# Kernel optimization log

Hardware: AMD Instinct MI355X
Metric: run time of the kernel (lower is better)

Reference implementation:

```python
import jax, jax.numpy as jnp
import jax.scipy.linalg as jsp
import numpy as np

# Problem dimensions (match init_kwargs P_shape/A_shape)
N = 256   # variables
M = 512   # constraints
B = 64    # batch

# OSQP ADMM hyper-parameters (fixed-rho variant of the OSQP algorithm)
SIGMA = 1e-6
RHO = 0.1
ALPHA = 1.6
N_ITERS = 500


def setup_inputs() -> dict:
    key = jax.random.key(0)
    kP, kq, kA, kc = jax.random.split(key, 4)
    # P is diagonal with strictly positive entries -> PSD (values are the nnz of P)
    P_val = jax.random.uniform(kP, (B, N), dtype=jnp.float32) + 0.1
    q_val = jax.random.normal(kq, (B, N), dtype=jnp.float32)
    # A is a dense pattern; values stored row-major as its nnz vector
    A_val = jax.random.normal(kA, (B, M * N), dtype=jnp.float32) / np.sqrt(N)
    # Feasible box: l <= u by construction
    center = jax.random.normal(kc, (B, M), dtype=jnp.float32)
    l_val = center - 1.0
    u_val = center + 1.0
    return {"P_val": P_val, "q_val": q_val, "A_val": A_val, "l_val": l_val, "u_val": u_val}


def _admm_qp(P_val, q_val, A_val, l_val, u_val):
    """Batched OSQP-style ADMM solve of min 1/2 x'Px + q'x  s.t. l <= Ax <= u.

    P is diagonal (nnz pattern = diag), A is dense (nnz pattern = full m x n).
    """
    A = A_val.reshape(B, M, N)                      # [B,m,n]
    # KKT-like matrix M_k = P + sigma*I + rho*A'A   [B,n,n]
    eye = jnp.eye(N, dtype=P_val.dtype)
    P_diag = P_val + SIGMA                          # diagonal of P + sigma*I
    Mk = RHO * jnp.einsum('bmi,bmj->bij', A, A) + jax.vmap(jnp.diag)(P_diag)
    L = jnp.linalg.cholesky(Mk)                     # [B,n,n], factor once, reuse
    Lt = jnp.swapaxes(L, -1, -2)

    def kkt_solve(rhs):                             # rhs [B,n]
        y1 = jsp.solve_triangular(L, rhs[..., None], lower=True)
        y2 = jsp.solve_triangular(Lt, y1, lower=False)
        return y2[..., 0]

    x0 = jnp.zeros((B, N), dtype=P_val.dtype)
    z0 = jnp.zeros((B, M), dtype=P_val.dtype)
    y0 = jnp.zeros((B, M), dtype=P_val.dtype)

    def step(state, _):
        x, z, y = state
        rhs = SIGMA * x - q_val + jnp.einsum('bmn,bm->bn', A, RHO * z - y)
        x_t = kkt_solve(rhs)                        # x-tilde
        z_t = jnp.einsum('bmn,bn->bm', A, x_t)      # z-tilde = A x_t
        x_new = ALPHA * x_t + (1.0 - ALPHA) * x
        z_hat = ALPHA * z_t + (1.0 - ALPHA) * z
        z_new = jnp.clip(z_hat + y / RHO, l_val, u_val)
        y_new = y + RHO * (z_hat - z_new)
        return (x_new, z_new, y_new), None

    (x, _, _), _ = jax.lax.scan(step, (x0, z0, y0), None, length=N_ITERS)
    return x


def reference(P_val, q_val, A_val, l_val, u_val):
    return _admm_qp(P_val, q_val, A_val, l_val, u_val)   # [B, n] primal solutions
```

## Files before the change

### kernel.cpp

```cpp
#include <hip/hip_runtime.h>
#include <hip/hip_fp16.h>

#define N_VAR 256
#define M_CON 512
#define BATCH 64
#define SIGMA_C 1e-6f
#define RHO_C 0.1f
#define ALPHA_C 1.6f
#define NITERS 500

typedef _Float16 f16x8 __attribute__((ext_vector_type(8)));
typedef float f32x4 __attribute__((ext_vector_type(4)));

__global__ __launch_bounds__(256) void k_transpose(const float* __restrict__ A,
                                                   float* __restrict__ At) {
  __shared__ float tile[32][33];
  int b = blockIdx.z;
  int n0 = blockIdx.x * 32;
  int m0 = blockIdx.y * 32;
  const float* Ab = A + (size_t)b * (M_CON * N_VAR);
  float* Atb = At + (size_t)b * (M_CON * N_VAR);
  int tx = threadIdx.x, ty = threadIdx.y;
#pragma unroll
  for (int j = 0; j < 32; j += 8)
    tile[ty + j][tx] = Ab[(size_t)(m0 + ty + j) * N_VAR + n0 + tx];
  __syncthreads();
#pragma unroll
  for (int j = 0; j < 32; j += 8)
    Atb[(size_t)(n0 + ty + j) * M_CON + m0 + tx] = tile[tx][ty + j];
}

__global__ __launch_bounds__(256) void k_ntgemm(
    const float* __restrict__ X, const float* __restrict__ Y,
    float* __restrict__ C, float* __restrict__ C2, int I, int J, int K,
    long long bsX, long long bsY, long long bsC, float alpha,
    const float* __restrict__ diagv, int tilesJ, int packC) {
  int b = blockIdx.y;
  int ti = blockIdx.x / tilesJ, tj = blockIdx.x % tilesJ;
  int i0 = ti * 128, j0 = tj * 128;
  const float* Xb = X + (size_t)b * bsX;
  const float* Yb = Y + (size_t)b * bsY;
  __shared__ float Xs[16][128];
  __shared__ float Ys[16][128];
  int tid = threadIdx.x;
  int tx = tid & 15, ty = tid >> 4;
  float acc[8][8];
#pragma unroll
  for (int r = 0; r < 8; ++r)
#pragma unroll
    for (int c = 0; c < 8; ++c) acc[r][c] = 0.0f;

  for (int kk = 0; kk < K; kk += 16) {
#pragma unroll
    for (int v = 0; v < 2; ++v) {
      int idx = v * 256 + tid;
      int row = idx >> 2;
      int k4 = (idx & 3) * 4;
      float4 gx = *(const float4*)(Xb + (size_t)(i0 + row) * K + kk + k4);
      Xs[k4 + 0][row] = gx.x; Xs[k4 + 1][row] = gx.y;
      Xs[k4 + 2][row] = gx.z; Xs[k4 + 3][row] = gx.w;
      float4 gy = *(const float4*)(Yb + (size_t)(j0 + row) * K + kk + k4);
      Ys[k4 + 0][row] = gy.x; Ys[k4 + 1][row] = gy.y;
      Ys[k4 + 2][row] = gy.z; Ys[k4 + 3][row] = gy.w;
    }
    __syncthreads();
#pragma unroll
    for (int k = 0; k < 16; ++k) {
      float xr[8], yr[8];
      *(float4*)&xr[0] = *(float4*)&Xs[k][ty * 8];
      *(float4*)&xr[4] = *(float4*)&Xs[k][ty * 8 + 4];
      *(float4*)&yr[0] = *(float4*)&Ys[k][tx * 8];
      *(float4*)&yr[4] = *(float4*)&Ys[k][tx * 8 + 4];
#pragma unroll
      for (int r = 0; r < 8; ++r)
#pragma unroll
        for (int c = 0; c < 8; ++c) acc[r][c] += xr[r] * yr[c];
    }
    __syncthreads();
  }
  if (packC == 2) {
    unsigned* Ch = (unsigned*)C + (size_t)b * 65536;
    unsigned* Ce = (unsigned*)C2 + (size_t)b * 65536;
#pragma unroll
    for (int r = 0; r < 8; ++r) {
      int gi = i0 + ty * 8 + r;
#pragma unroll
      for (int c = 0; c < 8; c += 2) {
        int gj = j0 + tx * 8 + c;
        float v0 = acc[r][c] * alpha, v1 = acc[r][c + 1] * alpha;
        __half2 hh = __floats2half2_rn(v0, v1);
        float2 fb = __half22float2(hh);
        __half2 he = __floats2half2_rn((v0 - fb.x) * 256.0f,
                                       (v1 - fb.y) * 256.0f);
        int idx = gi * 128 + (gj >> 1);
        Ch[idx] = *(unsigned*)&hh;
        Ce[idx] = *(unsigned*)&he;
      }
    }
    return;
  }
  float* Cb = C + (size_t)b * bsC;
#pragma unroll
  for (int r = 0; r < 8; ++r) {
    int gi = i0 + ty * 8 + r;
#pragma unroll
    for (int c = 0; c < 8; ++c) {
      int gj = j0 + tx * 8 + c;
      float val = acc[r][c] * alpha;
      if (diagv != nullptr && gi == gj) val += diagv[(size_t)b * N_VAR + gi] + SIGMA_C;
      Cb[(size_t)gi * J + gj] = val;
    }
  }
}

__global__ __launch_bounds__(256) void k_cast_split(
    const float* __restrict__ in, unsigned* __restrict__ oh,
    unsigned* __restrict__ oe, int n4) {
  int i = blockIdx.x * 256 + threadIdx.x;
  if (i >= n4) return;
  float4 v = ((const float4*)in)[i];
  __half2 h01 = __floats2half2_rn(v.x, v.y);
  __half2 h23 = __floats2half2_rn(v.z, v.w);
  float2 f01 = __half22float2(h01);
  float2 f23 = __half22float2(h23);
  __half2 e01 = __floats2half2_rn((v.x - f01.x) * 256.0f, (v.y - f01.y) * 256.0f);
  __half2 e23 = __floats2half2_rn((v.z - f23.x) * 256.0f, (v.w - f23.y) * 256.0f);
  uint2 uh; uh.x = *(unsigned*)&h01; uh.y = *(unsigned*)&h23;
  uint2 ue; ue.x = *(unsigned*)&e01; ue.y = *(unsigned*)&e23;
  ((uint2*)oh)[i] = uh;
  ((uint2*)oe)[i] = ue;
}

__global__ __launch_bounds__(256, 4) void k_mfma_g(
    const _Float16* __restrict__ Fh, const _Float16* __restrict__ Fe,
    const _Float16* __restrict__ Ah, const _Float16* __restrict__ Ae,
    unsigned* __restrict__ Gp) {
  int b = blockIdx.y;
  int bx = blockIdx.x;
  int t = threadIdx.x, l = t & 63, wv = t >> 6;
  int i0 = (bx >> 2) * 32;
  int j0 = (bx & 3) * 128 + wv * 32;
  const _Float16* Fhb = Fh + (size_t)b * 131072;
  const _Float16* Feb = Fe + (size_t)b * 131072;
  const _Float16* Ahb = Ah + (size_t)b * 131072;
  const _Float16* Aeb = Ae + (size_t)b * 131072;
  unsigned* Gpb = Gp + (size_t)b * 131072;

  int lr = l & 15, lk = (l >> 4) * 8;
  f32x4 acc00 = {0,0,0,0}, acc01 = {0,0,0,0}, acc10 = {0,0,0,0}, acc11 = {0,0,0,0};
  f32x4 ar00 = {0,0,0,0}, ar01 = {0,0,0,0}, ar10 = {0,0,0,0}, ar11 = {0,0,0,0};

  for (int kk = 0; kk < 256; kk += 32) {
    f16x8 af0 = *(const f16x8*)&Fhb[(size_t)(i0 + lr) * 256 + kk + lk];
    f16x8 af1 = *(const f16x8*)&Fhb[(size_t)(i0 + 16 + lr) * 256 + kk + lk];
    f16x8 ae0 = *(const f16x8*)&Feb[(size_t)(i0 + lr) * 256 + kk + lk];
    f16x8 ae1 = *(const f16x8*)&Feb[(size_t)(i0 + 16 + lr) * 256 + kk + lk];
    f16x8 bf0 = *(const f16x8*)&Ahb[(size_t)(j0 + lr) * 256 + kk + lk];
    f16x8 bf1 = *(const f16x8*)&Ahb[(size_t)(j0 + 16 + lr) * 256 + kk + lk];
    f16x8 be0 = *(const f16x8*)&Aeb[(size_t)(j0 + lr) * 256 + kk + lk];
    f16x8 be1 = *(const f16x8*)&Aeb[(size_t)(j0 + 16 + lr) * 256 + kk + lk];
    acc00 = __builtin_amdgcn_mfma_f32_16x16x32_f16(af0, bf0, acc00, 0, 0, 0);
    acc01 = __builtin_amdgcn_mfma_f32_16x16x32_f16(af0, bf1, acc01, 0, 0, 0);
    acc10 = __builtin_amdgcn_mfma_f32_16x16x32_f16(af1, bf0, acc10, 0, 0, 0);
    acc11 = __builtin_amdgcn_mfma_f32_16x16x32_f16(af1, bf1, acc11, 0, 0, 0);
    ar00 = __builtin_amdgcn_mfma_f32_16x16x32_f16(af0, be0, ar00, 0, 0, 0);
    ar01 = __builtin_amdgcn_mfma_f32_16x16x32_f16(af0, be1, ar01, 0, 0, 0);
    ar10 = __builtin_amdgcn_mfma_f32_16x16x32_f16(af1, be0, ar10, 0, 0, 0);
    ar11 = __builtin_amdgcn_mfma_f32_16x16x32_f16(af1, be1, ar11, 0, 0, 0);
    ar00 = __builtin_amdgcn_mfma_f32_16x16x32_f16(ae0, bf0, ar00, 0, 0, 0);
    ar01 = __builtin_amdgcn_mfma_f32_16x16x32_f16(ae0, bf1, ar01, 0, 0, 0);
    ar10 = __builtin_amdgcn_mfma_f32_16x16x32_f16(ae1, bf0, ar10, 0, 0, 0);
    ar11 = __builtin_amdgcn_mfma_f32_16x16x32_f16(ae1, bf1, ar11, 0, 0, 0);
  }

#pragma unroll
  for (int tr = 0; tr < 2; ++tr)
#pragma unroll
    for (int tc = 0; tc < 2; ++tc) {
      const f32x4* am = (tr == 0) ? ((tc == 0) ? &acc00 : &acc01)
                                  : ((tc == 0) ? &acc10 : &acc11);
      const f32x4* ae = (tr == 0) ? ((tc == 0) ? &ar00 : &ar01)
                                  : ((tc == 0) ? &ar10 : &ar11);
#pragma unroll
      for (int r = 0; r < 4; ++r) {
        float v = (*am)[r] + (*ae)[r] * (1.0f / 256.0f);
        float vp = __shfl_xor(v, 1);
        int gi = i0 + tr * 16 + (l >> 4) * 4 + r;
        int gj = j0 + tc * 16 + lr;
        if (!(l & 1)) {
          __half2 hh = __floats2half2_rn(v, vp);
          int sl = gi >> 7, rl = gi & 127;
          int t2 = ((((gj >> 7) << 1) | (rl >> 6)) << 6) | (rl & 63);
          Gpb[(size_t)sl * 32768 + ((gj & 127) >> 1) * 512 + t2] = *(unsigned*)&hh;
        }
      }
    }
}

__global__ __launch_bounds__(512, 2) void k_invert(const float* __restrict__ Mk,
                                                   float* __restrict__ Mi) {
  int b = blockIdx.x;
  const float* src = Mk + (size_t)b * 65536;
  float* dst = Mi + (size_t)b * 65536;
  int t = threadIdx.x;
  int c = t & 255, rh = t >> 8;

  float a[128];
#pragma unroll
  for (int j = 0; j < 128; ++j) a[j] = src[(size_t)(rh * 128 + j) * 256 + c];

  __shared__ float colPan[256][8];
  __shared__ float rowPan[2][8][260];
  __shared__ float PiSh[64];
  __shared__ float Rp[8][260];

  int rh_s = __builtin_amdgcn_readfirstlane(rh);
  int cw_s = __builtin_amdgcn_readfirstlane((t >> 6) & 3);

  if (rh == 0) {
#pragma unroll
    for (int j = 0; j < 8; ++j) rowPan[0][j][c] = a[j];
  }
  __syncthreads();

  for (int s = 0; s < 32; ++s) {
    int kb = s * 8;
    int cur = s & 1, nxt = cur ^ 1;
    int kh = kb >> 7, kj = kb & 127;
    int khn = (kb + 8) >> 7, kjn = (kb + 8) & 127;
    bool mycol = (c >= kb) && (c < kb + 8);

    if (cw_s == (kb >> 6)) {
      if (mycol) {
        int f = c - kb;
#pragma unroll
        for (int j = 0; j < 128; ++j) colPan[rh * 128 + j][f] = a[j];
      }
    }
    if (t < 64) {
      int e = t >> 3, f = t & 7;
      float p = rowPan[cur][e][kb + f];
#pragma unroll
      for (int k2 = 0; k2 < 8; ++k2) {
        float piv = __shfl(p, k2 * 8 + k2);
        float rv = __shfl(p, k2 * 8 + f);
        float cv = __shfl(p, e * 8 + k2);
        float pivinv = 1.0f / piv;
        float srv = rv * pivinv;
        float gen = p - cv * srv;
        p = gen;
        if (e == k2) p = srv;
        if (f == k2) p = -cv * pivinv;
        if (e == k2 && f == k2) p = pivinv;
      }
      PiSh[t] = p;
    }
    __syncthreads();

    float rpan[8];
#pragma unroll
    for (int f2 = 0; f2 < 8; ++f2) rpan[f2] = rowPan[cur][f2][c];
    float rp[8];
#pragma unroll
    for (int e = 0; e < 8; ++e) {
      float4 p0 = *(const float4*)&PiSh[e * 8];
      float4 p1 = *(const float4*)&PiSh[e * 8 + 4];
      rp[e] = p0.x * rpan[0] + p0.y * rpan[1] + p0.z * rpan[2] + p0.w * rpan[3] +
              p1.x * rpan[4] + p1.y * rpan[5] + p1.z * rpan[6] + p1.w * rpan[7];
    }
    if (cw_s == (kb >> 6)) {
      if (mycol) {
        int f = c - kb;
#pragma unroll
        for (int e = 0; e < 8; ++e) rp[e] = PiSh[e * 8 + f];
      }
    }
#pragma unroll
    for (int e = 0; e < 8; ++e) Rp[e][c] = rp[e];

    bool myhalfk = (rh_s == kh);
    bool stashw = (s != 31) && (rh_s == khn);
#pragma unroll
    for (int j = 0; j < 128; ++j) {
      float4 c0 = *(const float4*)&colPan[rh * 128 + j][0];
      float4 c1 = *(const float4*)&colPan[rh * 128 + j][4];
      float aold = a[j];
      float nv = aold -
                 (c0.x * rp[0] + c0.y * rp[1] + c0.z * rp[2] + c0.w * rp[3] +
                  c1.x * rp[4] + c1.y * rp[5] + c1.z * rp[6] + c1.w * rp[7]);
      if (mycol) nv -= aold;
      if (myhalfk && j >= kj && j < kj + 8)
        nv = Rp[j - kj][c];
      a[j] = nv;
      if (stashw && j >= kjn && j < kjn + 8)
        rowPan[nxt][j - kjn][c] = nv;
    }
    __syncthreads();
  }

#pragma unroll
  for (int j = 0; j < 128; ++j) dst[(size_t)(rh * 128 + j) * 256 + c] = a[j];
}

__global__ __launch_bounds__(256) void k_matvec_h(const float* __restrict__ Mi,
                                                  const float* __restrict__ q,
                                                  float* __restrict__ h) {
  int b = blockIdx.x, t = threadIdx.x;
  __shared__ float qs[256];
  qs[t] = q[(size_t)b * 256 + t];
  __syncthreads();
  const float* Mb = Mi + (size_t)b * 65536;
  float acc = 0.0f;
  for (int k = 0; k < 256; ++k) acc += Mb[(size_t)k * 256 + t] * qs[k];
  h[(size_t)b * 256 + t] = acc;
}

__global__ __launch_bounds__(512) void k_matvec_d(const float* __restrict__ At,
                                                  const float* __restrict__ h,
                                                  float* __restrict__ d) {
  int b = blockIdx.x, t = threadIdx.x;
  __shared__ float hs[256];
  if (t < 256) hs[t] = h[(size_t)b * 256 + t];
  __syncthreads();
  const float* Ab = At + (size_t)b * 131072;
  float acc = 0.0f;
  for (int n = 0; n < 256; ++n) acc += Ab[(size_t)n * 512 + t] * hs[n];
  d[(size_t)b * 512 + t] = acc;
}

__global__ __launch_bounds__(512) void k_admm4(
    const unsigned* __restrict__ Gpk_g, const float* __restrict__ dvec,
    const float* __restrict__ lv, const float* __restrict__ uv,
    unsigned long long* __restrict__ wtag, float* __restrict__ Sbuf) {
  int g = blockIdx.x;
  int b = (g & 7) + 8 * ((g >> 3) & 7);
  int s = g >> 6;
  int t = threadIdx.x;
  int l = t & 63, wv = t >> 6;
  int c0 = wv * 64;
  int cg = wv >> 1, hc = wv & 1;

  __shared__ __align__(16) float wbuf[8][64];
  __shared__ float part[2][8][128];

  const unsigned* gsrc =
      Gpk_g + (size_t)(b * 4 + s) * 32768 + (size_t)(hc * 32) * 512 + cg * 128 + l;

  float zreg = 0.0f, yreg = 0.0f, Sreg = 0.0f;
  float lreg = 0.0f, ureg = 0.0f, dreg = 0.0f;
  if (t < 128) {
    lreg = lv[(size_t)b * 512 + s * 128 + t];
    ureg = uv[(size_t)b * 512 + s * 128 + t];
    dreg = dvec[(size_t)b * 512 + s * 128 + t];
  }
  wbuf[wv][l] = 0.0f;

  unsigned long long* wt0 = wtag + (size_t)b * 512;
  unsigned long long* wt1 = wtag + 32768 + (size_t)b * 512;
  const float4* wq4 = (const float4*)(wbuf[wv]);

  for (int it = 0; it < NITERS; ++it) {
    unsigned gva[32], gvb[32];
#pragma unroll
    for (int k = 0; k < 32; ++k) {
      gva[k] = gsrc[(size_t)k * 512];
      gvb[k] = gsrc[(size_t)k * 512 + 64];
    }

    if (it > 0) {
      unsigned long long* wp = (it & 1) ? wt1 : wt0;
      unsigned want = (unsigned)it;
      unsigned long long v = __hip_atomic_load(&wp[c0 + l], __ATOMIC_RELAXED,
                                               __HIP_MEMORY_SCOPE_AGENT);
      bool got = ((unsigned)(v >> 32) == want);
      while (!__all(got)) {
        if (!got) {
          unsigned long long v2 = __hip_atomic_load(
              &wp[c0 + l], __ATOMIC_RELAXED, __HIP_MEMORY_SCOPE_AGENT);
          if ((unsigned)(v2 >> 32) == want) { v = v2; got = true; }
        }
      }
      wbuf[wv][l] = __uint_as_float((unsigned)(v & 0xffffffffu));
    }

    float r0a = 0.f, r0b = 0.f, r1a = 0.f, r1b = 0.f;
#pragma unroll
    for (int j = 0; j < 8; ++j) {
      float4 wa = wq4[2 * j];
      float4 wc = wq4[2 * j + 1];
      float2 fa0 = __half22float2(*(__half2*)&gva[4 * j + 0]);
      float2 fa1 = __half22float2(*(__half2*)&gva[4 * j + 1]);
      float2 fa2 = __half22float2(*(__half2*)&gva[4 * j + 2]);
      float2 fa3 = __half22float2(*(__half2*)&gva[4 * j + 3]);
      float2 fb0 = __half22float2(*(__half2*)&gvb[4 * j + 0]);
      float2 fb1 = __half22float2(*(__half2*)&gvb[4 * j + 1]);
      float2 fb2 = __half22float2(*(__half2*)&gvb[4 * j + 2]);
      float2 fb3 = __half22float2(*(__half2*)&gvb[4 * j + 3]);
      r0a += fa0.x * wa.x + fa0.y * wa.y + fa1.x * wa.z + fa1.y * wa.w;
      r0b += fa2.x * wc.x + fa2.y * wc.y + fa3.x * wc.z + fa3.y * wc.w;
      r1a += fb0.x * wa.x + fb0.y * wa.y + fb1.x * wa.z + fb1.y * wa.w;
      r1b += fb2.x * wc.x + fb2.y * wc.y + fb3.x * wc.z + fb3.y * wc.w;
    }
    int pp = it & 1;
    part[pp][wv][l] = r0a + r0b;
    part[pp][wv][64 + l] = r1a + r1b;
    __syncthreads();

    if (t < 128) {
      float w_old = RHO_C * zreg - yreg;
      Sreg = w_old - 0.6f * Sreg;
      float p = part[pp][0][t] + part[pp][1][t] + part[pp][2][t] +
                part[pp][3][t] + part[pp][4][t] + part[pp][5][t] +
                part[pp][6][t] + part[pp][7][t];
      float zt = p - dreg;
      float zh = ALPHA_C * zt + (1.0f - ALPHA_C) * zreg;
      float zc = zh + yreg * (1.0f / RHO_C);
      zc = fminf(fmaxf(zc, lreg), ureg);
      yreg += RHO_C * (zh - zc);
      zreg = zc;
      if (it < NITERS - 1) {
        float wn = RHO_C * zreg - yreg;
        unsigned long long pk =
            ((unsigned long long)(unsigned)(it + 1) << 32) |
            (unsigned long long)__float_as_uint(wn);
        unsigned long long* wp = ((it + 1) & 1) ? wt1 : wt0;
        __hip_atomic_store(&wp[s * 128 + t], pk, __ATOMIC_RELAXED,
                           __HIP_MEMORY_SCOPE_AGENT);
      }
    }
  }

  if (t < 128) Sbuf[(size_t)b * 512 + s * 128 + t] = Sreg;
}

__global__ __launch_bounds__(256) void k_final(
    const float* __restrict__ A, const float* __restrict__ q,
    const float* __restrict__ Mi, const float* __restrict__ Sbuf,
    float* __restrict__ xout) {
  int b = blockIdx.x, t = threadIdx.x;
  __shared__ float Ssh[512];
  __shared__ float uu[256];
  for (int i = t; i < 512; i += 256) Ssh[i] = Sbuf[(size_t)b * 512 + i];
  __syncthreads();
  const float* Ab = A + (size_t)b * 131072;
  float acc = 0.0f;
  for (int m = 0; m < 512; ++m) acc += Ab[(size_t)m * 256 + t] * Ssh[m];
  uu[t] = ALPHA_C * acc - q[(size_t)b * 256 + t];
  __syncthreads();
  const float* Mb = Mi + (size_t)b * 65536;
  float x = 0.0f;
  for (int kk = 0; kk < 256; ++kk) x += Mb[(size_t)kk * 256 + t] * uu[kk];
  xout[(size_t)b * 256 + t] = x;
}

extern "C" void kernel_launch(void* const* d_in, const int* in_sizes, int n_in,
                              void* d_out, int out_size, void* d_ws, size_t ws_size,
                              hipStream_t stream) {
  (void)in_sizes; (void)n_in; (void)out_size; (void)ws_size;
  const float* P = (const float*)d_in[0];
  const float* q = (const float*)d_in[1];
  const float* Av = (const float*)d_in[2];
  const float* lv = (const float*)d_in[3];
  const float* uv = (const float*)d_in[4];
  float* xout = (float*)d_out;

  float* ws = (float*)d_ws;
  float* At = ws;
  unsigned* Ah = (unsigned*)ws;
  unsigned* Ae = (unsigned*)(ws + 4194304);
  float* Mi = ws + 8388608;
  float* Mk = ws + 12582912;
  float* Gp = ws + 12582912;
  float* Fh = ws + 20971520;
  float* Fe = ws + 25165824;
  float* hv = ws + 29360128;
  float* dv = ws + 29376512;
  float* Sbuf = ws + 29409280;
  unsigned long long* wtag = (unsigned long long*)(ws + 29442048);

  hipMemsetAsync(wtag, 0, 131072 * 4, stream);

  k_transpose<<<dim3(8, 16, 64), dim3(32, 8), 0, stream>>>(Av, At);
  k_ntgemm<<<dim3(4, 64), 256, 0, stream>>>(At, At, Mk, nullptr, 256, 256, 512,
                                            131072LL, 131072LL, 65536LL,
                                            RHO_C, P, 2, 0);
  k_invert<<<64, 512, 0, stream>>>(Mk, Mi);
  k_matvec_h<<<64, 256, 0, stream>>>(Mi, q, hv);
  k_matvec_d<<<64, 512, 0, stream>>>(At, hv, dv);
  k_cast_split<<<8192, 256, 0, stream>>>(Av, Ah, Ae, 2097152);
  k_ntgemm<<<dim3(8, 64), 256, 0, stream>>>(Av, Mi, Fh, Fe, 512, 256, 256,
                                            131072LL, 65536LL, 0LL,
                                            1.0f, nullptr, 2, 2);
  k_mfma_g<<<dim3(64, 64), 256, 0, stream>>>(
      (const _Float16*)Fh, (const _Float16*)Fe,
      (const _Float16*)Ah, (const _Float16*)Ae, (unsigned*)Gp);
  k_admm4<<<256, 512, 0, stream>>>((const unsigned*)Gp, dv, lv, uv, wtag, Sbuf);
  k_final<<<64, 256, 0, stream>>>(Av, q, Mi, Sbuf, xout);
}
```

Before: 1.539 ms.

## Cache half of the G block in LDS and vectorize remaining global loads

The precomputed G matrix is split into two halves with a new per-thread contiguous layout. In the persistent ADMM kernel, one half is loaded once into 64KB of shared memory and reused across all iterations. The other half is streamed from global memory each iteration as wide uint4 loads instead of 64 scalar strided loads. This cuts per-iteration global/L2 traffic in the latency-bound loop, at the cost of large LDS usage, which limits blocks per CU.

```diff
diff --git a/kernel.cpp b/kernel.cpp
--- a/kernel.cpp
+++ b/kernel.cpp
@@ -134,7 +134,7 @@
 __global__ __launch_bounds__(256, 4) void k_mfma_g(
     const _Float16* __restrict__ Fh, const _Float16* __restrict__ Fe,
     const _Float16* __restrict__ Ah, const _Float16* __restrict__ Ae,
-    unsigned* __restrict__ Gp) {
+    unsigned* __restrict__ GA, unsigned* __restrict__ GB) {
   int b = blockIdx.y;
   int bx = blockIdx.x;
   int t = threadIdx.x, l = t & 63, wv = t >> 6;
@@ -144,7 +144,6 @@
   const _Float16* Feb = Fe + (size_t)b * 131072;
   const _Float16* Ahb = Ah + (size_t)b * 131072;
   const _Float16* Aeb = Ae + (size_t)b * 131072;
-  unsigned* Gpb = Gp + (size_t)b * 131072;
 
   int lr = l & 15, lk = (l >> 4) * 8;
   f32x4 acc00 = {0,0,0,0}, acc01 = {0,0,0,0}, acc10 = {0,0,0,0}, acc11 = {0,0,0,0};
@@ -190,8 +189,11 @@
         if (!(l & 1)) {
           __half2 hh = __floats2half2_rn(v, vp);
           int sl = gi >> 7, rl = gi & 127;
-          int t2 = ((((gj >> 7) << 1) | (rl >> 6)) << 6) | (rl & 63);
-          Gpb[(size_t)sl * 32768 + ((gj & 127) >> 1) * 512 + t2] = *(unsigned*)&hh;
+          size_t idx =
+              ((size_t)((b * 4 + sl) * 512 + (gj >> 6) * 64 + (rl & 63))) * 32 +
+              ((gj >> 1) & 31);
+          if (rl & 64) GB[idx] = *(unsigned*)&hh;
+          else         GA[idx] = *(unsigned*)&hh;
         }
       }
     }
@@ -329,22 +331,30 @@
 }
 
 __global__ __launch_bounds__(512) void k_admm4(
-    const unsigned* __restrict__ Gpk_g, const float* __restrict__ dvec,
-    const float* __restrict__ lv, const float* __restrict__ uv,
-    unsigned long long* __restrict__ wtag, float* __restrict__ Sbuf) {
+    const unsigned* __restrict__ GA, const unsigned* __restrict__ GB,
+    const float* __restrict__ dvec, const float* __restrict__ lv,
+    const float* __restrict__ uv, unsigned long long* __restrict__ wtag,
+    float* __restrict__ Sbuf) {
   int g = blockIdx.x;
   int b = (g & 7) + 8 * ((g >> 3) & 7);
   int s = g >> 6;
   int t = threadIdx.x;
   int l = t & 63, wv = t >> 6;
   int c0 = wv * 64;
-  int cg = wv >> 1, hc = wv & 1;
-
+
+  __shared__ __align__(16) unsigned Gs[16384];
   __shared__ __align__(16) float wbuf[8][64];
   __shared__ float part[2][8][128];
 
-  const unsigned* gsrc =
-      Gpk_g + (size_t)(b * 4 + s) * 32768 + (size_t)(hc * 32) * 512 + cg * 128 + l;
+  const uint4* gA =
+      (const uint4*)(GA + ((size_t)(b * 4 + s) * 512 + c0 + l) * 32);
+  const uint4* gB =
+      (const uint4*)(GB + ((size_t)(b * 4 + s) * 512 + c0 + l) * 32);
+  uint4* GsV = (uint4*)Gs;
+
+#pragma unroll
+  for (int j4 = 0; j4 < 8; ++j4)
+    GsV[(wv * 8 + j4) * 64 + l] = gA[j4];
 
   float zreg = 0.0f, yreg = 0.0f, Sreg = 0.0f;
   float lreg = 0.0f, ureg = 0.0f, dreg = 0.0f;
@@ -360,12 +370,9 @@
   const float4* wq4 = (const float4*)(wbuf[wv]);
 
   for (int it = 0; it < NITERS; ++it) {
-    unsigned gva[32], gvb[32];
-#pragma unroll
-    for (int k = 0; k < 32; ++k) {
-      gva[k] = gsrc[(size_t)k * 512];
-      gvb[k] = gsrc[(size_t)k * 512 + 64];
-    }
+    uint4 gb[8];
+#pragma unroll
+    for (int k = 0; k < 8; ++k) gb[k] = gB[k];
 
     if (it > 0) {
       unsigned long long* wp = (it & 1) ? wt1 : wt0;
@@ -388,14 +395,16 @@
     for (int j = 0; j < 8; ++j) {
       float4 wa = wq4[2 * j];
       float4 wc = wq4[2 * j + 1];
-      float2 fa0 = __half22float2(*(__half2*)&gva[4 * j + 0]);
-      float2 fa1 = __half22float2(*(__half2*)&gva[4 * j + 1]);
-      float2 fa2 = __half22float2(*(__half2*)&gva[4 * j + 2]);
-      float2 fa3 = __half22float2(*(__half2*)&gva[4 * j + 3]);
-      float2 fb0 = __half22float2(*(__half2*)&gvb[4 * j + 0]);
-      float2 fb1 = __half22float2(*(__half2*)&gvb[4 * j + 1]);
-      float2 fb2 = __half22float2(*(__half2*)&gvb[4 * j + 2]);
-      float2 fb3 = __half22float2(*(__half2*)&gvb[4 * j + 3]);
+      uint4 ga = GsV[(wv * 8 + j) * 64 + l];
+      uint4 gv = gb[j];
+      float2 fa0 = __half22float2(*(__half2*)&ga.x);
+      float2 fa1 = __half22float2(*(__half2*)&ga.y);
+      float2 fa2 = __half22float2(*(__half2*)&ga.z);
+      float2 fa3 = __half22float2(*(__half2*)&ga.w);
+      float2 fb0 = __half22float2(*(__half2*)&gv.x);
+      float2 fb1 = __half22float2(*(__half2*)&gv.y);
+      float2 fb2 = __half22float2(*(__half2*)&gv.z);
+      float2 fb3 = __half22float2(*(__half2*)&gv.w);
       r0a += fa0.x * wa.x + fa0.y * wa.y + fa1.x * wa.z + fa1.y * wa.w;
       r0b += fa2.x * wc.x + fa2.y * wc.y + fa3.x * wc.z + fa3.y * wc.w;
       r1a += fb0.x * wa.x + fb0.y * wa.y + fb1.x * wa.z + fb1.y * wa.w;
@@ -470,7 +479,8 @@
   unsigned* Ae = (unsigned*)(ws + 4194304);
   float* Mi = ws + 8388608;
   float* Mk = ws + 12582912;
-  float* Gp = ws + 12582912;
+  unsigned* GA = (unsigned*)(ws + 12582912);
+  unsigned* GB = (unsigned*)(ws + 16777216);
   float* Fh = ws + 20971520;
   float* Fe = ws + 25165824;
   float* hv = ws + 29360128;
@@ -493,7 +503,7 @@
                                             1.0f, nullptr, 2, 2);
   k_mfma_g<<<dim3(64, 64), 256, 0, stream>>>(
       (const _Float16*)Fh, (const _Float16*)Fe,
-      (const _Float16*)Ah, (const _Float16*)Ae, (unsigned*)Gp);
-  k_admm4<<<256, 512, 0, stream>>>((const unsigned*)Gp, dv, lv, uv, wtag, Sbuf);
+      (const _Float16*)Ah, (const _Float16*)Ae, GA, GB);
+  k_admm4<<<256, 512, 0, stream>>>(GA, GB, dv, lv, uv, wtag, Sbuf);
   k_final<<<64, 256, 0, stream>>>(Av, q, Mi, Sbuf, xout);
 }
```

Measured after the change: 1.641 ms. 1.07x slower.

## Replace FP32 SIMT GEMMs with split-FP16 MFMA GEMMs for setup stages

Applied to the files above, without the earlier changes.

Removes the scalar-FP32 tiled GEMM kernel and computes A'A and A*Minv with a new MFMA kernel. The kernel splits each operand into a high FP16 part and a scaled residual part, then recombines three cross products to recover near-FP32 accuracy. This adds cast-split passes over At and Mi and reshuffles workspace buffers to hold them. Separately, the ADMM loop now loads the G-matrix values inside the inner loop instead of prefetching them into 64 registers, which lowers register pressure but exposes load latency after the wait. The emulated precision may differ slightly from true FP32.

```diff
diff --git a/kernel.cpp b/kernel.cpp
--- a/kernel.cpp
+++ b/kernel.cpp
@@ -28,89 +28,6 @@
 #pragma unroll
   for (int j = 0; j < 32; j += 8)
     Atb[(size_t)(n0 + ty + j) * M_CON + m0 + tx] = tile[tx][ty + j];
-}
-
-__global__ __launch_bounds__(256) void k_ntgemm(
-    const float* __restrict__ X, const float* __restrict__ Y,
-    float* __restrict__ C, float* __restrict__ C2, int I, int J, int K,
-    long long bsX, long long bsY, long long bsC, float alpha,
-    const float* __restrict__ diagv, int tilesJ, int packC) {
-  int b = blockIdx.y;
-  int ti = blockIdx.x / tilesJ, tj = blockIdx.x % tilesJ;
-  int i0 = ti * 128, j0 = tj * 128;
-  const float* Xb = X + (size_t)b * bsX;
-  const float* Yb = Y + (size_t)b * bsY;
-  __shared__ float Xs[16][128];
-  __shared__ float Ys[16][128];
-  int tid = threadIdx.x;
-  int tx = tid & 15, ty = tid >> 4;
-  float acc[8][8];
-#pragma unroll
-  for (int r = 0; r < 8; ++r)
-#pragma unroll
-    for (int c = 0; c < 8; ++c) acc[r][c] = 0.0f;
-
-  for (int kk = 0; kk < K; kk += 16) {
-#pragma unroll
-    for (int v = 0; v < 2; ++v) {
-      int idx = v * 256 + tid;
-      int row = idx >> 2;
-      int k4 = (idx & 3) * 4;
-      float4 gx = *(const float4*)(Xb + (size_t)(i0 + row) * K + kk + k4);
-      Xs[k4 + 0][row] = gx.x; Xs[k4 + 1][row] = gx.y;
-      Xs[k4 + 2][row] = gx.z; Xs[k4 + 3][row] = gx.w;
-      float4 gy = *(const float4*)(Yb + (size_t)(j0 + row) * K + kk + k4);
-      Ys[k4 + 0][row] = gy.x; Ys[k4 + 1][row] = gy.y;
-      Ys[k4 + 2][row] = gy.z; Ys[k4 + 3][row] = gy.w;
-    }
-    __syncthreads();
-#pragma unroll
-    for (int k = 0; k < 16; ++k) {
-      float xr[8], yr[8];
-      *(float4*)&xr[0] = *(float4*)&Xs[k][ty * 8];
-      *(float4*)&xr[4] = *(float4*)&Xs[k][ty * 8 + 4];
-      *(float4*)&yr[0] = *(float4*)&Ys[k][tx * 8];
-      *(float4*)&yr[4] = *(float4*)&Ys[k][tx * 8 + 4];
-#pragma unroll
-      for (int r = 0; r < 8; ++r)
-#pragma unroll
-        for (int c = 0; c < 8; ++c) acc[r][c] += xr[r] * yr[c];
-    }
-    __syncthreads();
-  }
-  if (packC == 2) {
-    unsigned* Ch = (unsigned*)C + (size_t)b * 65536;
-    unsigned* Ce = (unsigned*)C2 + (size_t)b * 65536;
-#pragma unroll
-    for (int r = 0; r < 8; ++r) {
-      int gi = i0 + ty * 8 + r;
-#pragma unroll
-      for (int c = 0; c < 8; c += 2) {
-        int gj = j0 + tx * 8 + c;
-        float v0 = acc[r][c] * alpha, v1 = acc[r][c + 1] * alpha;
-        __half2 hh = __floats2half2_rn(v0, v1);
-        float2 fb = __half22float2(hh);
-        __half2 he = __floats2half2_rn((v0 - fb.x) * 256.0f,
-                                       (v1 - fb.y) * 256.0f);
-        int idx = gi * 128 + (gj >> 1);
-        Ch[idx] = *(unsigned*)&hh;
-        Ce[idx] = *(unsigned*)&he;
-      }
-    }
-    return;
-  }
-  float* Cb = C + (size_t)b * bsC;
-#pragma unroll
-  for (int r = 0; r < 8; ++r) {
-    int gi = i0 + ty * 8 + r;
-#pragma unroll
-    for (int c = 0; c < 8; ++c) {
-      int gj = j0 + tx * 8 + c;
-      float val = acc[r][c] * alpha;
-      if (diagv != nullptr && gi == gj) val += diagv[(size_t)b * N_VAR + gi] + SIGMA_C;
-      Cb[(size_t)gi * J + gj] = val;
-    }
-  }
 }
 
 __global__ __launch_bounds__(256) void k_cast_split(
@@ -129,6 +46,81 @@
   uint2 ue; ue.x = *(unsigned*)&e01; ue.y = *(unsigned*)&e23;
   ((uint2*)oh)[i] = uh;
   ((uint2*)oe)[i] = ue;
+}
+
+__global__ __launch_bounds__(256, 4) void k_mfma_nt(
+    const _Float16* __restrict__ Xh, const _Float16* __restrict__ Xe,
+    const _Float16* __restrict__ Yh, const _Float16* __restrict__ Ye,
+    float* __restrict__ C0, float* __restrict__ C1,
+    int K, int jTiles, long long bsX, long long bsY, long long bsC,
+    float alpha, const float* __restrict__ diagv, int mode) {
+  int b = blockIdx.y;
+  int bx = blockIdx.x;
+  int t = threadIdx.x, l = t & 63, wv = t >> 6;
+  int i0 = (bx / jTiles) * 32;
+  int j0 = (bx % jTiles) * 128 + wv * 32;
+  const _Float16* Xhb = Xh + (size_t)b * bsX;
+  const _Float16* Xeb = Xe + (size_t)b * bsX;
+  const _Float16* Yhb = Yh + (size_t)b * bsY;
+  const _Float16* Yeb = Ye + (size_t)b * bsY;
+
+  int lr = l & 15, lk = (l >> 4) * 8;
+  f32x4 m00 = {0,0,0,0}, m01 = {0,0,0,0}, m10 = {0,0,0,0}, m11 = {0,0,0,0};
+  f32x4 c00 = {0,0,0,0}, c01 = {0,0,0,0}, c10 = {0,0,0,0}, c11 = {0,0,0,0};
+  f32x4 s00 = {0,0,0,0}, s01 = {0,0,0,0}, s10 = {0,0,0,0}, s11 = {0,0,0,0};
+
+  for (int kk = 0; kk < K; kk += 32) {
+    f16x8 xh0 = *(const f16x8*)&Xhb[(size_t)(i0 + lr) * K + kk + lk];
+    f16x8 xh1 = *(const f16x8*)&Xhb[(size_t)(i0 + 16 + lr) * K + kk + lk];
+    f16x8 xe0 = *(const f16x8*)&Xeb[(size_t)(i0 + lr) * K + kk + lk];
+    f16x8 xe1 = *(const f16x8*)&Xeb[(size_t)(i0 + 16 + lr) * K + kk + lk];
+    f16x8 yh0 = *(const f16x8*)&Yhb[(size_t)(j0 + lr) * K + kk + lk];
+    f16x8 yh1 = *(const f16x8*)&Yhb[(size_t)(j0 + 16 + lr) * K + kk + lk];
+    f16x8 ye0 = *(const f16x8*)&Yeb[(size_t)(j0 + lr) * K + kk + lk];
+    f16x8 ye1 = *(const f16x8*)&Yeb[(size_t)(j0 + 16 + lr) * K + kk + lk];
+    m00 = __builtin_amdgcn_mfma_f32_16x16x32_f16(xh0, yh0, m00, 0, 0, 0);
+    m01 = __builtin_amdgcn_mfma_f32_16x16x32_f16(xh0, yh1, m01, 0, 0, 0);
+    m10 = __builtin_amdgcn_mfma_f32_16x16x32_f16(xh1, yh0, m10, 0, 0, 0);
+    m11 = __builtin_amdgcn_mfma_f32_16x16x32_f16(xh1, yh1, m11, 0, 0, 0);
+    c00 = __builtin_amdgcn_mfma_f32_16x16x32_f16(xh0, ye0, c00, 0, 0, 0);
+    c01 = __builtin_amdgcn_mfma_f32_16x16x32_f16(xh0, ye1, c01, 0, 0, 0);
+    c10 = __builtin_amdgcn_mfma_f32_16x16x32_f16(xh1, ye0, c10, 0, 0, 0);
+    c11 = __builtin_amdgcn_mfma_f32_16x16x32_f16(xh1, ye1, c11, 0, 0, 0);
+    c00 = __builtin_amdgcn_mfma_f32_16x16x32_f16(xe0, yh0, c00, 0, 0, 0);
+    c01 = __builtin_amdgcn_mfma_f32_16x16x32_f16(xe0, yh1, c01, 0, 0, 0);
+    c10 = __builtin_amdgcn_mfma_f32_16x16x32_f16(xe1, yh0, c10, 0, 0, 0);
+    c11 = __builtin_amdgcn_mfma_f32_16x16x32_f16(xe1, yh1, c11, 0, 0, 0);
+    s00 = __builtin_amdgcn_mfma_f32_16x16x32_f16(xe0, ye0, s00, 0, 0, 0);
+    s01 = __builtin_amdgcn_mfma_f32_16x16x32_f16(xe0, ye1, s01, 0, 0, 0);
+    s10 = __builtin_amdgcn_mfma_f32_16x16x32_f16(xe1, ye0, s10, 0, 0, 0);
+    s11 = __builtin_amdgcn_mfma_f32_16x16x32_f16(xe1, ye1, s11, 0, 0, 0);
+  }
+
+#pragma unroll
+  for (int tr = 0; tr < 2; ++tr)
+#pragma unroll
+    for (int tc = 0; tc < 2; ++tc) {
+      f32x4 vm = tr ? (tc ? m11 : m10) : (tc ? m01 : m00);
+      f32x4 vc = tr ? (tc ? c11 : c10) : (tc ? c01 : c00);
+      f32x4 vs = tr ? (tc ? s11 : s10) : (tc ? s01 : s00);
+#pragma unroll
+      for (int r = 0; r < 4; ++r) {
+        float v = (vm[r] + vc[r] * (1.0f / 256.0f) +
+                   vs[r] * (1.0f / 65536.0f)) * alpha;
+        int gi = i0 + tr * 16 + (l >> 4) * 4 + r;
+        int gj = j0 + tc * 16 + lr;
+        if (mode == 0) {
+          if (diagv != nullptr && gi == gj)
+            v += diagv[(size_t)b * N_VAR + gi] + SIGMA_C;
+          C0[(size_t)b * bsC + (size_t)gi * 256 + gj] = v;
+        } else {
+          _Float16 fh = (_Float16)v;
+          _Float16 fe = (_Float16)((v - (float)fh) * 256.0f);
+          ((_Float16*)C0)[(size_t)b * bsC + (size_t)gi * 256 + gj] = fh;
+          ((_Float16*)C1)[(size_t)b * bsC + (size_t)gi * 256 + gj] = fe;
+        }
+      }
+    }
 }
 
 __global__ __launch_bounds__(256, 4) void k_mfma_g(
@@ -360,13 +352,6 @@
   const float4* wq4 = (const float4*)(wbuf[wv]);
 
   for (int it = 0; it < NITERS; ++it) {
-    unsigned gva[32], gvb[32];
-#pragma unroll
-    for (int k = 0; k < 32; ++k) {
-      gva[k] = gsrc[(size_t)k * 512];
-      gvb[k] = gsrc[(size_t)k * 512 + 64];
-    }
-
     if (it > 0) {
       unsigned long long* wp = (it & 1) ? wt1 : wt0;
       unsigned want = (unsigned)it;
@@ -388,14 +373,22 @@
     for (int j = 0; j < 8; ++j) {
       float4 wa = wq4[2 * j];
       float4 wc = wq4[2 * j + 1];
-      float2 fa0 = __half22float2(*(__half2*)&gva[4 * j + 0]);
-      float2 fa1 = __half22float2(*(__half2*)&gva[4 * j + 1]);
-      float2 fa2 = __half22float2(*(__half2*)&gva[4 * j + 2]);
-      float2 fa3 = __half22float2(*(__half2*)&gva[4 * j + 3]);
-      float2 fb0 = __half22float2(*(__half2*)&gvb[4 * j + 0]);
-      float2 fb1 = __half22float2(*(__half2*)&gvb[4 * j + 1]);
-      float2 fb2 = __half22float2(*(__half2*)&gvb[4 * j + 2]);
-      float2 fb3 = __half22float2(*(__half2*)&gvb[4 * j + 3]);
+      unsigned a0 = gsrc[(4 * j + 0) * 512];
+      unsigned a1 = gsrc[(4 * j + 1) * 512];
+      unsigned a2 = gsrc[(4 * j + 2) * 512];
+      unsigned a3 = gsrc[(4 * j + 3) * 512];
+      unsigned b0 = gsrc[(4 * j + 0) * 512 + 64];
+      unsigned b1 = gsrc[(4 * j + 1) * 512 + 64];
+      unsigned b2 = gsrc[(4 * j + 2) * 512 + 64];
+      unsigned b3 = gsrc[(4 * j + 3) * 512 + 64];
+      float2 fa0 = __half22float2(*(__half2*)&a0);
+      float2 fa1 = __half22float2(*(__half2*)&a1);
+      float2 fa2 = __half22float2(*(__half2*)&a2);
+      float2 fa3 = __half22float2(*(__half2*)&a3);
+      float2 fb0 = __half22float2(*(__half2*)&b0);
+      float2 fb1 = __half22float2(*(__half2*)&b1);
+      float2 fb2 = __half22float2(*(__half2*)&b2);
+      float2 fb3 = __half22float2(*(__half2*)&b3);
       r0a += fa0.x * wa.x + fa0.y * wa.y + fa1.x * wa.z + fa1.y * wa.w;
       r0b += fa2.x * wc.x + fa2.y * wc.y + fa3.x * wc.z + fa3.y * wc.w;
       r1a += fb0.x * wa.x + fb0.y * wa.y + fb1.x * wa.z + fb1.y * wa.w;
@@ -466,34 +459,42 @@
 
   float* ws = (float*)d_ws;
   float* At = ws;
-  unsigned* Ah = (unsigned*)ws;
-  unsigned* Ae = (unsigned*)(ws + 4194304);
+  float* Fh = ws;
+  float* Fe = ws + 4194304;
   float* Mi = ws + 8388608;
   float* Mk = ws + 12582912;
-  float* Gp = ws + 12582912;
-  float* Fh = ws + 20971520;
-  float* Fe = ws + 25165824;
+  unsigned* Mih = (unsigned*)(ws + 12582912);
+  unsigned* Mie = (unsigned*)(ws + 14680064);
+  unsigned* Gp = (unsigned*)(ws + 12582912);
+  unsigned* Ath = (unsigned*)(ws + 20971520);
+  unsigned* Ate = (unsigned*)(ws + 25165824);
+  unsigned* Ah = (unsigned*)(ws + 20971520);
+  unsigned* Ae = (unsigned*)(ws + 25165824);
   float* hv = ws + 29360128;
   float* dv = ws + 29376512;
   float* Sbuf = ws + 29409280;
   unsigned long long* wtag = (unsigned long long*)(ws + 29442048);
 
-  hipMemsetAsync(wtag, 0, 131072 * 4, stream);
+  hipMemsetAsync(wtag, 0, 524288, stream);
 
   k_transpose<<<dim3(8, 16, 64), dim3(32, 8), 0, stream>>>(Av, At);
-  k_ntgemm<<<dim3(4, 64), 256, 0, stream>>>(At, At, Mk, nullptr, 256, 256, 512,
-                                            131072LL, 131072LL, 65536LL,
-                                            RHO_C, P, 2, 0);
+  k_cast_split<<<8192, 256, 0, stream>>>(At, Ath, Ate, 2097152);
+  k_mfma_nt<<<dim3(16, 64), 256, 0, stream>>>(
+      (const _Float16*)Ath, (const _Float16*)Ate,
+      (const _Float16*)Ath, (const _Float16*)Ate,
+      Mk, nullptr, 512, 2, 131072LL, 131072LL, 65536LL, RHO_C, P, 0);
   k_invert<<<64, 512, 0, stream>>>(Mk, Mi);
   k_matvec_h<<<64, 256, 0, stream>>>(Mi, q, hv);
   k_matvec_d<<<64, 512, 0, stream>>>(At, hv, dv);
   k_cast_split<<<8192, 256, 0, stream>>>(Av, Ah, Ae, 2097152);
-  k_ntgemm<<<dim3(8, 64), 256, 0, stream>>>(Av, Mi, Fh, Fe, 512, 256, 256,
-                                            131072LL, 65536LL, 0LL,
-                                            1.0f, nullptr, 2, 2);
+  k_cast_split<<<4096, 256, 0, stream>>>(Mi, Mih, Mie, 1048576);
+  k_mfma_nt<<<dim3(32, 64), 256, 0, stream>>>(
+      (const _Float16*)Ah, (const _Float16*)Ae,
+      (const _Float16*)Mih, (const _Float16*)Mie,
+      Fh, Fe, 256, 2, 131072LL, 65536LL, 131072LL, 1.0f, nullptr, 1);
   k_mfma_g<<<dim3(64, 64), 256, 0, stream>>>(
       (const _Float16*)Fh, (const _Float16*)Fe,
-      (const _Float16*)Ah, (const _Float16*)Ae, (unsigned*)Gp);
-  k_admm4<<<256, 512, 0, stream>>>((const unsigned*)Gp, dv, lv, uv, wtag, Sbuf);
+      (const _Float16*)Ah, (const _Float16*)Ae, Gp);
+  k_admm4<<<256, 512, 0, stream>>>(Gp, dv, lv, uv, wtag, Sbuf);
   k_final<<<64, 256, 0, stream>>>(Av, q, Mi, Sbuf, xout);
 }
```

Measured after the change: 1.557 ms. Within noise of the previous version (+1.1%).
